# Optimization experiments

Hardware: AMD Instinct MI355X
Metric: run time of the kernel (lower is better)

## Reference

```python
import jax, jax.numpy as jnp
import numpy as np

B, T, I, H, O = 128, 500, 512, 1024, 11
BETA, THRESH, GAMMA, SPARSITY = 0.9, 1.0, 0.5, 0.05

@jax.custom_vjp
def spike(x):
    return (x > 0).astype(x.dtype)

def _spike_fwd(x):
    return (x > 0).astype(x.dtype), x

def _spike_bwd(x, g):
    # surrogate gradient: gamma / (1 + |x|)^2
    return (g * GAMMA / jnp.square(1.0 + jnp.abs(x)),)

spike.defvjp(_spike_fwd, _spike_bwd)


def setup_inputs() -> dict:
    key = jax.random.key(0)
    k0, k1, k2, k3, k4 = jax.random.split(key, 5)
    x = jax.random.normal(k0, (B, T, I), jnp.float32)
    # xavier-uniform-like init for W_in / W_out, orthogonal-ish (scaled normal) for W_rec
    lim_in = (6.0 / (I + H)) ** 0.5
    lim_out = (6.0 / (H + O)) ** 0.5
    W_in = jax.random.uniform(k1, (I, H), jnp.float32, -lim_in, lim_in)
    W_rec = jax.random.normal(k2, (H, H), jnp.float32) / jnp.sqrt(jnp.float32(H))
    W_out = jax.random.uniform(k3, (H, O), jnp.float32, -lim_out, lim_out)
    # fixed sparse connectivity mask: Bernoulli(sparsity), no self-connections
    mask = (jax.random.uniform(k4, (H, H)) < SPARSITY).astype(jnp.float32)
    mask = mask * (1.0 - jnp.eye(H, dtype=jnp.float32))
    W_rec = W_rec * mask  # reset_parameters() applies mask at init when mask is not learnable
    h_bias = jnp.zeros((H,), jnp.float32)
    b_out = jnp.zeros((O,), jnp.float32)
    return {"x": x, "W_in": W_in, "W_rec": W_rec, "W_out": W_out,
            "h_bias": h_bias, "b_out": b_out, "mask": mask}


def reference(x, W_in, W_rec, W_out, h_bias, b_out, mask):
    W_eff = W_rec * mask                                   # masked recurrent weights [H,H]
    drive = jnp.einsum('bti,ih->bth', x, W_in) + h_bias    # per-step input drive [B,T,H]
    drive_t = jnp.swapaxes(drive, 0, 1)                    # [T,B,H]

    def step(carry, d_t):
        v, s = carry
        v = BETA * v + d_t + s @ W_eff                     # LIF membrane update
        s_new = spike(v - THRESH)                          # surrogate threshold spike
        v = v - jax.lax.stop_gradient(s_new) * THRESH      # subtract reset (detached)
        out_t = s_new @ W_out + b_out                      # per-step readout [B,O]
        return (v, s_new), out_t

    init = (jnp.zeros((x.shape[0], W_eff.shape[0]), x.dtype),
            jnp.zeros((x.shape[0], W_eff.shape[0]), x.dtype))
    _, outs = jax.lax.scan(step, init, drive_t)            # outs: [T,B,O]
    return jnp.mean(outs, axis=0)                          # 'rate' readout -> [B,O]
```

## Files before the change

kernel.cpp:

```cpp
#include <hip/hip_runtime.h>
#include <cstdint>
#include <cstddef>

#define B_ 128
#define T_ 500
#define I_ 512
#define H_ 1024
#define O_ 11
#define BETA 0.9f
#define THRESH 1.0f
#define K2_ 1536
#define LDA 72

typedef __attribute__((ext_vector_type(4))) float f32x4;
typedef __attribute__((ext_vector_type(8))) short bf16x8;
typedef __attribute__((ext_vector_type(4))) unsigned int u32x4;

struct ScanSmem {
  int accL[H_];
  unsigned int listL[H_];
  unsigned int fcL[2];
  float red[H_];
  float part[352];
};
struct GemmSmem {
  alignas(16) unsigned short As[128 * LDA];
  alignas(16) unsigned short Bs[256 * LDA];
};
union FusedSmem { ScanSmem s; GemmSmem g; };

__device__ __forceinline__ unsigned short bf16_rne(float f) {
  unsigned int u = __float_as_uint(f);
  unsigned int r = u + 0x7FFFu + ((u >> 16) & 1u);
  return (unsigned short)(r >> 16);
}
__device__ __forceinline__ float bf16_to_f(unsigned short h) {
  return __uint_as_float(((unsigned int)h) << 16);
}

__global__ void k_csr(const float* __restrict__ W_rec, const float* __restrict__ mask,
                      unsigned int* __restrict__ csr, unsigned int* __restrict__ rowhi) {
  int r = blockIdx.x * 4 + (threadIdx.x >> 6);
  int lane = threadIdx.x & 63;
  unsigned cnt = 0;
  const float* mrow = mask + (size_t)r * H_;
  const float* wrow = W_rec + (size_t)r * H_;
  for (int c = 0; c < 16; ++c) {
    float m = mrow[c * 64 + lane];
    bool nz = (m != 0.f);
    unsigned long long bb = __ballot(nz);
    unsigned pos = cnt + (unsigned)__popcll(bb & ((1ull << lane) - 1ull));
    if (nz) {
      float w = wrow[c * 64 + lane] * m;
      int wi = __float2int_rn(w * 8388608.f);
      wi = wi > 2097151 ? 2097151 : (wi < -2097151 ? -2097151 : wi);
      if (pos < 128u) csr[((size_t)r << 7) + pos] = (((unsigned)wi) << 10) | (unsigned)(c * 64 + lane);
    }
    cnt += (unsigned)__popcll(bb);
  }
  for (unsigned p = (cnt > 128u ? 128u : cnt) + (unsigned)lane; p < 128u; p += 64u)
    csr[((size_t)r << 7) + p] = (p & 63u);
  if (lane == 0) rowhi[r] = (cnt > 64u) ? 1u : 0u;
}

__global__ void k_build_wt(const float* __restrict__ W_in, unsigned short* __restrict__ Wt) {
  int n = blockIdx.y;
  int k2 = blockIdx.x * 256 + threadIdx.x;
  int i = k2 & 511;
  int c = k2 >> 9;
  float w = W_in[i * H_ + n];
  unsigned short hi = bf16_rne(w);
  unsigned short v = (c == 2) ? bf16_rne(w - bf16_to_f(hi)) : hi;
  Wt[(size_t)n * K2_ + k2] = v;
}

__device__ __forceinline__ void gemm_body(const float* __restrict__ x,
                                          const unsigned short* __restrict__ Wt,
                                          float* __restrict__ drive, int t0, int Tc,
                                          int id, int tid,
                                          unsigned short* As, unsigned short* Bs) {
  int mt = (id >> 5) * 8 + (id & 7);
  int nt = (id >> 3) & 3;
  if (mt >= Tc) return;
  int lane = tid & 63, w = tid >> 6;
  int wr = w >> 3, wc = w & 7;
  f32x4 acc[4][2] = {};
  int arow = tid >> 3, aoct = tid & 7;
  int brow = tid >> 2, bq = tid & 3;
  int rr = mt * 128 + arow;
  int bb = rr / Tc, tt = rr - bb * Tc;
  const float* xrow = x + ((size_t)(bb * T_ + t0 + tt)) * I_ + aoct * 8;
  const unsigned short* wtrow = Wt + (size_t)(nt * 256 + brow) * K2_ + bq * 16;
  for (int kt = 0; kt < K2_ / 64; ++kt) {
    int creg = kt >> 3;
    const float* ap = xrow + (kt & 7) * 64;
    float4 a0 = *(const float4*)(ap);
    float4 a1 = *(const float4*)(ap + 4);
    u32x4 b0 = *(const u32x4*)(wtrow + kt * 64);
    u32x4 b1 = *(const u32x4*)(wtrow + kt * 64 + 8);
    alignas(16) unsigned short o[8];
    float vv[8] = {a0.x, a0.y, a0.z, a0.w, a1.x, a1.y, a1.z, a1.w};
#pragma unroll
    for (int j = 0; j < 8; ++j) {
      unsigned short hi = bf16_rne(vv[j]);
      o[j] = (creg == 1) ? bf16_rne(vv[j] - bf16_to_f(hi)) : hi;
    }
    __syncthreads();
    *(u32x4*)&As[arow * LDA + aoct * 8] = *(u32x4*)o;
    *(u32x4*)&Bs[brow * LDA + bq * 16] = b0;
    *(u32x4*)&Bs[brow * LDA + bq * 16 + 8] = b1;
    __syncthreads();
#pragma unroll
    for (int kk = 0; kk < 2; ++kk) {
      bf16x8 af[4], bf[2];
#pragma unroll
      for (int mi = 0; mi < 4; ++mi)
        af[mi] = *(const bf16x8*)&As[(wr * 64 + mi * 16 + (lane & 15)) * LDA + kk * 32 + (lane >> 4) * 8];
#pragma unroll
      for (int ni = 0; ni < 2; ++ni)
        bf[ni] = *(const bf16x8*)&Bs[(wc * 32 + ni * 16 + (lane & 15)) * LDA + kk * 32 + (lane >> 4) * 8];
#pragma unroll
      for (int mi = 0; mi < 4; ++mi)
#pragma unroll
        for (int ni = 0; ni < 2; ++ni)
          acc[mi][ni] = __builtin_amdgcn_mfma_f32_16x16x32_bf16(af[mi], bf[ni], acc[mi][ni], 0, 0, 0);
    }
  }
  int r0 = (lane >> 4) * 4, c0 = lane & 15;
#pragma unroll
  for (int mi = 0; mi < 4; ++mi) {
    int rowb = mt * 128 + wr * 64 + mi * 16 + r0;
#pragma unroll
    for (int ni = 0; ni < 2; ++ni) {
      int col = nt * 256 + wc * 32 + ni * 16 + c0;
#pragma unroll
      for (int r = 0; r < 4; ++r)
        drive[(size_t)(rowb + r) * H_ + col] = acc[mi][ni][r];
    }
  }
}

__global__ __launch_bounds__(1024, 1) void k_gemm(const float* __restrict__ x,
                                                  const unsigned short* __restrict__ Wt,
                                                  float* __restrict__ drive, int t0, int Tc) {
  __shared__ GemmSmem g;
  gemm_body(x, Wt, drive, t0, Tc, blockIdx.x, threadIdx.x, g.As, g.Bs);
}

__device__ __forceinline__ void step_one(
    float dcur, int cur, int tid, int lane, unsigned wvu, unsigned myhi, float bias,
    const unsigned int* __restrict__ csr, int* accL, unsigned int* listL, unsigned int* fcL,
    float& v, float& s, float& cnt) {
  unsigned F = (unsigned)__builtin_amdgcn_readfirstlane((int)fcL[cur]);
  unsigned lo = (F * wvu) >> 4;
  unsigned hi = (F * (wvu + 1u)) >> 4;
  for (unsigned i0 = lo; i0 < hi; i0 += 8u) {
    unsigned idx = i0 + ((unsigned)lane & 7u);
    unsigned packed = listL[idx < hi ? idx : (hi - 1u)];
#define EDECL(n) unsigned e##n = (i0 + n##u < hi) ? (unsigned)__builtin_amdgcn_readlane((int)packed, n) : 1024u; \
                 unsigned ea##n = 0u, eb##n = 0u;
    EDECL(0) EDECL(1) EDECL(2) EDECL(3) EDECL(4) EDECL(5) EDECL(6) EDECL(7)
#undef EDECL
#define ELOAD(n) if (e##n != 1024u) { \
      const unsigned int* rp = csr + ((size_t)(e##n & 1023u) << 7); \
      ea##n = rp[lane]; \
      if (e##n & 4096u) eb##n = rp[64 + lane]; }
    ELOAD(0) ELOAD(1) ELOAD(2) ELOAD(3) ELOAD(4) ELOAD(5) ELOAD(6) ELOAD(7)
#undef ELOAD
#define EATOM(n) if (e##n != 1024u) { \
      atomicAdd(&accL[ea##n & 1023u], ((int)ea##n) >> 10); \
      if (e##n & 4096u) atomicAdd(&accL[eb##n & 1023u], ((int)eb##n) >> 10); }
    EATOM(0) EATOM(1) EATOM(2) EATOM(3) EATOM(4) EATOM(5) EATOM(6) EATOM(7)
#undef EATOM
  }
  __syncthreads();
  int ri = accL[tid];
  accL[tid] = 0;
  v = BETA * v + (dcur + bias) + (float)ri * 1.1920929e-7f;
  bool f = v > THRESH;
  v -= f ? THRESH : 0.f;
  cnt += f ? 1.f : 0.f;
  s = f ? 1.f : 0.f;
  unsigned long long bb = __ballot(f);
  unsigned n = (unsigned)__popcll(bb);
  unsigned pos = (unsigned)__popcll(bb & ((1ull << lane) - 1ull));
  unsigned wb = 0;
  if (lane == 0) wb = atomicAdd(&fcL[cur ^ 1], n);
  wb = (unsigned)__builtin_amdgcn_readfirstlane((int)wb);
  if (f) listL[wb + pos] = (unsigned)tid | myhi;
  if (tid == 0) fcL[cur] = 0;
  __syncthreads();
}

__device__ __forceinline__ void scan_body(
    const float* __restrict__ drive, const unsigned int* __restrict__ csr,
    const unsigned int* __restrict__ rowhi,
    const float* __restrict__ h_bias, const float* __restrict__ W_out,
    const float* __restrict__ b_out,
    float* __restrict__ state_v, float* __restrict__ state_s, float* __restrict__ state_c,
    float* __restrict__ out, int t0, int Tc, int last, int b, int tid, ScanSmem& sm) {
  int lane = tid & 63;
  unsigned wvu = (unsigned)__builtin_amdgcn_readfirstlane(tid >> 6);
  float bias = h_bias[tid];
  unsigned myhi = rowhi[tid] << 12;
  float v, s, cnt;
  if (t0 == 0) { v = 0.f; s = 0.f; cnt = 0.f; }
  else { v = state_v[b * H_ + tid]; s = state_s[b * H_ + tid]; cnt = state_c[b * H_ + tid]; }
  sm.accL[tid] = 0;
  if (tid < 2) sm.fcL[tid] = 0;
  __syncthreads();
  {
    bool f0 = s > 0.f;
    unsigned long long bb = __ballot(f0);
    unsigned n = (unsigned)__popcll(bb);
    unsigned pos = (unsigned)__popcll(bb & ((1ull << lane) - 1ull));
    unsigned wb = 0;
    if (lane == 0) wb = atomicAdd(&sm.fcL[0], n);
    wb = (unsigned)__builtin_amdgcn_readfirstlane((int)wb);
    if (f0) sm.listL[wb + pos] = (unsigned)tid | myhi;
  }
  __syncthreads();
  const float* dptr = drive + (size_t)b * Tc * H_ + tid;
  for (int t8 = 0; t8 < Tc; t8 += 8) {
    float dd0 = (t8 + 0 < Tc) ? dptr[(size_t)(t8 + 0) * H_] : 0.f;
    float dd1 = (t8 + 1 < Tc) ? dptr[(size_t)(t8 + 1) * H_] : 0.f;
    float dd2 = (t8 + 2 < Tc) ? dptr[(size_t)(t8 + 2) * H_] : 0.f;
    float dd3 = (t8 + 3 < Tc) ? dptr[(size_t)(t8 + 3) * H_] : 0.f;
    float dd4 = (t8 + 4 < Tc) ? dptr[(size_t)(t8 + 4) * H_] : 0.f;
    float dd5 = (t8 + 5 < Tc) ? dptr[(size_t)(t8 + 5) * H_] : 0.f;
    float dd6 = (t8 + 6 < Tc) ? dptr[(size_t)(t8 + 6) * H_] : 0.f;
    float dd7 = (t8 + 7 < Tc) ? dptr[(size_t)(t8 + 7) * H_] : 0.f;
#define STEP(s_) if (t8 + s_ < Tc) \
    step_one(dd##s_, (s_ & 1), tid, lane, wvu, myhi, bias, csr, sm.accL, sm.listL, sm.fcL, v, s, cnt);
    STEP(0) STEP(1) STEP(2) STEP(3) STEP(4) STEP(5) STEP(6) STEP(7)
#undef STEP
  }
  if (!last) {
    state_v[b * H_ + tid] = v; state_s[b * H_ + tid] = s; state_c[b * H_ + tid] = cnt;
  } else {
    sm.red[tid] = cnt;
    __syncthreads();
    if (tid < 352) {
      int o = tid >> 5, seg = tid & 31;
      float p = 0.f;
      for (int j = 0; j < 32; ++j) {
        int hh = seg * 32 + j;
        p += sm.red[hh] * W_out[hh * O_ + o];
      }
      sm.part[tid] = p;
    }
    __syncthreads();
    if (tid < O_) {
      float sum = 0.f;
      for (int g = 0; g < 32; ++g) sum += sm.part[(tid << 5) + g];
      out[b * O_ + tid] = b_out[tid] + sum * (1.0f / (float)T_);
    }
  }
}

__global__ __launch_bounds__(1024, 1) void k_rsnn(
    const float* __restrict__ drive, const unsigned int* __restrict__ csr,
    const unsigned int* __restrict__ rowhi,
    const float* __restrict__ h_bias, const float* __restrict__ W_out,
    const float* __restrict__ b_out,
    float* __restrict__ state_v, float* __restrict__ state_s, float* __restrict__ state_c,
    float* __restrict__ out, int t0, int Tc, int last) {
  __shared__ ScanSmem sm;
  scan_body(drive, csr, rowhi, h_bias, W_out, b_out, state_v, state_s, state_c, out,
            t0, Tc, last, blockIdx.x, threadIdx.x, sm);
}

__global__ __launch_bounds__(1024, 1) void k_fused(
    const float* __restrict__ drive_s, const unsigned int* __restrict__ csr,
    const unsigned int* __restrict__ rowhi,
    const float* __restrict__ h_bias, const float* __restrict__ W_out,
    const float* __restrict__ b_out,
    float* __restrict__ state_v, float* __restrict__ state_s, float* __restrict__ state_c,
    float* __restrict__ out, int t0s, int Tcs,
    const float* __restrict__ x, const unsigned short* __restrict__ Wt,
    float* __restrict__ drive_g, int t0g, int Tcg) {
  __shared__ FusedSmem sm;
  if (blockIdx.x < 128) {
    scan_body(drive_s, csr, rowhi, h_bias, W_out, b_out, state_v, state_s, state_c, out,
              t0s, Tcs, 0, blockIdx.x, threadIdx.x, sm.s);
  } else {
    gemm_body(x, Wt, drive_g, t0g, Tcg, blockIdx.x - 128, threadIdx.x, sm.g.As, sm.g.Bs);
  }
}

extern "C" void kernel_launch(void* const* d_in, const int* in_sizes, int n_in,
                              void* d_out, int out_size, void* d_ws, size_t ws_size,
                              hipStream_t stream) {
  (void)in_sizes; (void)n_in; (void)out_size;
  const float* x = (const float*)d_in[0];
  const float* W_in = (const float*)d_in[1];
  const float* W_rec = (const float*)d_in[2];
  const float* W_out = (const float*)d_in[3];
  const float* h_bias = (const float*)d_in[4];
  const float* b_out = (const float*)d_in[5];
  const float* mask = (const float*)d_in[6];
  float* out = (float*)d_out;

  char* ws = (char*)d_ws;
  size_t off = 0;
  auto alloc = [&](size_t bytes) {
    void* p = ws + off;
    off = (off + bytes + 255) & ~(size_t)255;
    return p;
  };
  unsigned short* Wt = (unsigned short*)alloc((size_t)H_ * K2_ * 2);
  unsigned int* csr = (unsigned int*)alloc((size_t)H_ * 128 * 4);
  unsigned int* rowhi = (unsigned int*)alloc((size_t)H_ * 4);
  float* st_v = (float*)alloc((size_t)B_ * H_ * 4);
  float* st_s = (float*)alloc((size_t)B_ * H_ * 4);
  float* st_c = (float*)alloc((size_t)B_ * H_ * 4);
  size_t fixed = off;

  size_t avail = ws_size > fixed ? ws_size - fixed : 0;
  const size_t per_t = (size_t)128 * 1024 * 4;
  int TC = 128;
  while (TC > 1 && 2u * (size_t)TC * per_t > avail) TC >>= 1;
  float* driveA = (float*)alloc((size_t)TC * per_t);
  float* driveB = (float*)alloc((size_t)TC * per_t);
  int C = (T_ + TC - 1) / TC;

  k_csr<<<dim3(256), dim3(256), 0, stream>>>(W_rec, mask, csr, rowhi);
  k_build_wt<<<dim3(6, 1024), dim3(256), 0, stream>>>(W_in, Wt);

  {
    int tc0 = T_ < TC ? T_ : TC;
    k_gemm<<<dim3(((tc0 + 7) / 8) * 32), dim3(1024), 0, stream>>>(x, Wt, driveA, 0, tc0);
  }
  for (int c = 0; c < C; ++c) {
    int t0 = c * TC;
    int tc = (T_ - t0) < TC ? (T_ - t0) : TC;
    float* bufS = (c & 1) ? driveB : driveA;
    if (c + 1 < C) {
      int t0n = (c + 1) * TC;
      int tcn = (T_ - t0n) < TC ? (T_ - t0n) : TC;
      float* bufG = ((c + 1) & 1) ? driveB : driveA;
      int gblocks = ((tcn + 7) / 8) * 32;
      k_fused<<<dim3(128 + gblocks), dim3(1024), 0, stream>>>(
          bufS, csr, rowhi, h_bias, W_out, b_out, st_v, st_s, st_c, out, t0, tc,
          x, Wt, bufG, t0n, tcn);
    } else {
      k_rsnn<<<dim3(128), dim3(1024), 0, stream>>>(bufS, csr, rowhi, h_bias, W_out, b_out,
                                                   st_v, st_s, st_c, out, t0, tc, 1);
    }
  }
}
```

Baseline: 862.5 us.

## Use geometrically growing time chunks and merge prep kernels into one launch

Replaces the fixed 128-step chunking of the drive GEMM/scan pipeline with chunks that start at 24 steps and grow by 1.5x up to a workspace-bounded cap. This shrinks the unoverlapped first GEMM and the serial pipeline startup while keeping later chunks large. It also merges the CSR build and the W_in bf16 split into one kernel to save a launch. More chunks mean more fused-kernel launches, and the small early chunks give less GEMM work to overlap with each scan.

Result: slower. 889.0 us (+3.1%).

```diff
diff --git a/kernel.cpp b/kernel.cpp
--- a/kernel.cpp
+++ b/kernel.cpp
@@ -38,40 +38,45 @@
   return __uint_as_float(((unsigned int)h) << 16);
 }
 
-__global__ void k_csr(const float* __restrict__ W_rec, const float* __restrict__ mask,
-                      unsigned int* __restrict__ csr, unsigned int* __restrict__ rowhi) {
-  int r = blockIdx.x * 4 + (threadIdx.x >> 6);
-  int lane = threadIdx.x & 63;
-  unsigned cnt = 0;
-  const float* mrow = mask + (size_t)r * H_;
-  const float* wrow = W_rec + (size_t)r * H_;
-  for (int c = 0; c < 16; ++c) {
-    float m = mrow[c * 64 + lane];
-    bool nz = (m != 0.f);
-    unsigned long long bb = __ballot(nz);
-    unsigned pos = cnt + (unsigned)__popcll(bb & ((1ull << lane) - 1ull));
-    if (nz) {
-      float w = wrow[c * 64 + lane] * m;
-      int wi = __float2int_rn(w * 8388608.f);
-      wi = wi > 2097151 ? 2097151 : (wi < -2097151 ? -2097151 : wi);
-      if (pos < 128u) csr[((size_t)r << 7) + pos] = (((unsigned)wi) << 10) | (unsigned)(c * 64 + lane);
-    }
-    cnt += (unsigned)__popcll(bb);
-  }
-  for (unsigned p = (cnt > 128u ? 128u : cnt) + (unsigned)lane; p < 128u; p += 64u)
-    csr[((size_t)r << 7) + p] = (p & 63u);
-  if (lane == 0) rowhi[r] = (cnt > 64u) ? 1u : 0u;
-}
-
-__global__ void k_build_wt(const float* __restrict__ W_in, unsigned short* __restrict__ Wt) {
-  int n = blockIdx.y;
-  int k2 = blockIdx.x * 256 + threadIdx.x;
-  int i = k2 & 511;
-  int c = k2 >> 9;
-  float w = W_in[i * H_ + n];
-  unsigned short hi = bf16_rne(w);
-  unsigned short v = (c == 2) ? bf16_rne(w - bf16_to_f(hi)) : hi;
-  Wt[(size_t)n * K2_ + k2] = v;
+__global__ void k_prep(const float* __restrict__ W_rec, const float* __restrict__ mask,
+                       const float* __restrict__ W_in,
+                       unsigned int* __restrict__ csr, unsigned int* __restrict__ rowhi,
+                       unsigned short* __restrict__ Wt) {
+  int id = blockIdx.x;
+  int tid = threadIdx.x;
+  if (id < 256) {
+    int r = id * 4 + (tid >> 6);
+    int lane = tid & 63;
+    unsigned cnt = 0;
+    const float* mrow = mask + (size_t)r * H_;
+    const float* wrow = W_rec + (size_t)r * H_;
+    for (int c = 0; c < 16; ++c) {
+      float m = mrow[c * 64 + lane];
+      bool nz = (m != 0.f);
+      unsigned long long bb = __ballot(nz);
+      unsigned pos = cnt + (unsigned)__popcll(bb & ((1ull << lane) - 1ull));
+      if (nz) {
+        float w = wrow[c * 64 + lane] * m;
+        int wi = __float2int_rn(w * 8388608.f);
+        wi = wi > 2097151 ? 2097151 : (wi < -2097151 ? -2097151 : wi);
+        if (pos < 128u) csr[((size_t)r << 7) + pos] = (((unsigned)wi) << 10) | (unsigned)(c * 64 + lane);
+      }
+      cnt += (unsigned)__popcll(bb);
+    }
+    for (unsigned p = (cnt > 128u ? 128u : cnt) + (unsigned)lane; p < 128u; p += 64u)
+      csr[((size_t)r << 7) + p] = (p & 63u);
+    if (lane == 0) rowhi[r] = (cnt > 64u) ? 1u : 0u;
+  } else {
+    int wid = id - 256;
+    int n = wid / 6, kblk = wid - n * 6;
+    int k2 = kblk * 256 + tid;
+    int i = k2 & 511;
+    int c = k2 >> 9;
+    float w = W_in[i * H_ + n];
+    unsigned short hi = bf16_rne(w);
+    unsigned short v = (c == 2) ? bf16_rne(w - bf16_to_f(hi)) : hi;
+    Wt[(size_t)n * K2_ + k2] = v;
+  }
 }
 
 __device__ __forceinline__ void gemm_body(const float* __restrict__ x,
@@ -318,26 +323,38 @@
 
   size_t avail = ws_size > fixed ? ws_size - fixed : 0;
   const size_t per_t = (size_t)128 * 1024 * 4;
-  int TC = 128;
-  while (TC > 1 && 2u * (size_t)TC * per_t > avail) TC >>= 1;
-  float* driveA = (float*)alloc((size_t)TC * per_t);
-  float* driveB = (float*)alloc((size_t)TC * per_t);
-  int C = (T_ + TC - 1) / TC;
-
-  k_csr<<<dim3(256), dim3(256), 0, stream>>>(W_rec, mask, csr, rowhi);
-  k_build_wt<<<dim3(6, 1024), dim3(256), 0, stream>>>(W_in, Wt);
+  int tcmax = (int)(avail / (2 * per_t));
+  if (tcmax > 192) tcmax = 192;
+  if (tcmax < 8) tcmax = 8;
+  float* driveA = (float*)alloc((size_t)tcmax * per_t);
+  float* driveB = (float*)alloc((size_t)tcmax * per_t);
+
+  int sizes[64];
+  int C = 0, left = T_, sgrow = 24;
+  if (sgrow > tcmax) sgrow = tcmax;
+  while (left > 0 && C < 64) {
+    int take;
+    int absorb = sgrow * 2 < tcmax ? sgrow * 2 : tcmax;
+    if (left <= absorb) take = left < tcmax ? left : tcmax;
+    else take = sgrow;
+    sizes[C++] = take;
+    left -= take;
+    sgrow = sgrow + sgrow / 2;
+    if (sgrow > tcmax) sgrow = tcmax;
+  }
+  int starts[64];
+  { int t = 0; for (int c = 0; c < C; ++c) { starts[c] = t; t += sizes[c]; } }
+
+  k_prep<<<dim3(256 + 6 * 1024), dim3(256), 0, stream>>>(W_rec, mask, W_in, csr, rowhi, Wt);
 
   {
-    int tc0 = T_ < TC ? T_ : TC;
-    k_gemm<<<dim3(((tc0 + 7) / 8) * 32), dim3(1024), 0, stream>>>(x, Wt, driveA, 0, tc0);
+    k_gemm<<<dim3(((sizes[0] + 7) / 8) * 32), dim3(1024), 0, stream>>>(x, Wt, driveA, 0, sizes[0]);
   }
   for (int c = 0; c < C; ++c) {
-    int t0 = c * TC;
-    int tc = (T_ - t0) < TC ? (T_ - t0) : TC;
+    int t0 = starts[c], tc = sizes[c];
     float* bufS = (c & 1) ? driveB : driveA;
     if (c + 1 < C) {
-      int t0n = (c + 1) * TC;
-      int tcn = (T_ - t0n) < TC ? (T_ - t0n) : TC;
+      int t0n = starts[c + 1], tcn = sizes[c + 1];
       float* bufG = ((c + 1) & 1) ? driveB : driveA;
       int gblocks = ((tcn + 7) / 8) * 32;
       k_fused<<<dim3(128 + gblocks), dim3(1024), 0, stream>>>(
```
